# Kernel optimization log

Measured on AMD Instinct MI355X. Metric: run time of the kernel, lower is better.

## Reference

```python
import jax, jax.numpy as jnp
import numpy as np
from jax.scipy.linalg import solve_triangular

JITTER = 1e-5
BIG = 1e9


def _rq(d2, outscale, ls, alpha):
    # Rational-quadratic kernel (gpytorch RQKernel with outputscale)
    return outscale * (1.0 + d2 / (2.0 * alpha * ls * ls)) ** (-alpha)


def _per_var(tb, m, nz, os_, ls, al, K):
    # tb: [L] times of one sample; m: [L] bool, points belonging to this variable.
    # Sequential GP fantasy updates == prefix conditioning. chol of a leading
    # principal block equals leading block of full chol, so one Cholesky +
    # one triangular solve + cumsum over rows reproduces the sequential loop.
    L = tb.shape[0]
    keyt = jnp.where(m, tb, BIG)
    order = jnp.argsort(keyt)            # this variable's points, time-sorted, first
    ts = tb[order]
    ms = m[order]
    mf = ms.astype(tb.dtype)
    d2 = (ts[:, None] - ts[None, :]) ** 2
    Kxx = _rq(d2, os_, ls, al) * (mf[:, None] * mf[None, :])  # masked rows/cols -> 0
    idx = jnp.arange(L)
    # noisy train covariance; masked points get identity rows (decoupled, zero effect)
    Kn = Kxx.at[idx, idx].set(jnp.where(ms, os_ + nz + JITTER, 1.0))
    C = jnp.linalg.cholesky(Kn)
    v = solve_triangular(C, Kxx, lower=True)     # [L train, L test] (test = same points)
    cum = jnp.cumsum(v * v, axis=0)              # variance explained after i obs
    std_pref = jnp.sqrt(jnp.maximum(os_ - cum, 1e-12)) * mf[None, :]
    sums = std_pref.sum(axis=1)                  # sum of posterior stds after each obs
    s0 = jnp.sqrt(os_) * mf.sum()                # prior sum of stds
    prev = jnp.concatenate([s0[None], sums[:-1]])
    gains = jnp.maximum(prev - sums, 0.0) * mf   # info gain per added observation
    # partition timeline into K groups of near-equal total information
    cg = jnp.cumsum(gains)
    frac = (cg - 0.5 * gains) / jnp.maximum(cg[-1], 1e-12)
    grp = jnp.clip(jnp.floor(frac * K), 0, K - 1).astype(jnp.int32)
    return order, mf, grp, gains


def _forward(t, vid, noise, outputscale, lengthscale, alpha, K):
    B, L = t.shape
    V = noise.shape[0]

    def per_bv(tb, vidb, v):
        m = vidb == v
        order, mf, grp, gains = _per_var(tb, m, noise[v], outputscale[v],
                                         lengthscale[v], alpha[v], K)
        col = v * K + grp
        oh = jnp.zeros((L, V * K), t.dtype).at[order, col].add(mf)
        g = jnp.zeros((L,), t.dtype).at[order].add(gains)
        return oh, g

    def per_b(tb, vidb):
        oh, g = jax.vmap(per_bv, in_axes=(None, None, 0))(tb, vidb, jnp.arange(V))
        return oh.sum(0), g.sum(0)   # variables are disjoint -> sum == union

    return jax.vmap(per_b)(t, vid)


def setup_inputs() -> dict:
    key = jax.random.key(0)
    ks = jax.random.split(key, 7)
    B, L, V = 8, 512, 16
    t = jax.random.uniform(ks[0], (B, L), dtype=jnp.float32)
    y = jax.random.normal(ks[1], (B, L), dtype=jnp.float32)
    vid = jax.random.randint(ks[2], (B, L), 0, V, dtype=jnp.int32)
    noise = 0.01 + 0.05 * jax.random.uniform(ks[3], (V,), dtype=jnp.float32)
    outputscale = 0.5 + jax.random.uniform(ks[4], (V,), dtype=jnp.float32)
    lengthscale = 0.05 + 0.2 * jax.random.uniform(ks[5], (V,), dtype=jnp.float32)
    alpha = 0.5 + jax.random.uniform(ks[6], (V,), dtype=jnp.float32)
    return {"t": t, "y": y, "vid": vid, "noise": noise, "outputscale": outputscale,
            "lengthscale": lengthscale, "alpha": alpha, "hyper_num_nodes": 8}


def reference(t, y, vid, noise, outputscale, lengthscale, alpha, hyper_num_nodes):
    # Returns (mask [B, L, V*K] hard one-hot aggregation mask, gains [B, L] info gain).
    # GP posterior variance does not depend on y, so y only affects training (not here).
    mask, gains = _forward(t, vid, noise, outputscale, lengthscale, alpha, hyper_num_nodes)
    return mask, gains
```

## Files before the change

### kernel.cpp

```cpp
#include <hip/hip_runtime.h>
#include <math.h>

#define NMAX 64
#define JITTER 1e-5


__device__ __forceinline__ double rdlane_f64(double x, int lane) {
    union { double d; int i[2]; } a, r;
    a.d = x;
    r.i[0] = __builtin_amdgcn_readlane(a.i[0], lane);
    r.i[1] = __builtin_amdgcn_readlane(a.i[1], lane);
    return r.d;
}

#define FOR16(M) M(0) M(1) M(2) M(3) M(4) M(5) M(6) M(7) \
                 M(8) M(9) M(10) M(11) M(12) M(13) M(14) M(15)

#define FOR16_J(M, Kc) \
    M(Kc,0)  M(Kc,1)  M(Kc,2)  M(Kc,3)  M(Kc,4)  M(Kc,5)  M(Kc,6)  M(Kc,7) \
    M(Kc,8)  M(Kc,9)  M(Kc,10) M(Kc,11) M(Kc,12) M(Kc,13) M(Kc,14) M(Kc,15)

#define LOADT(j) \
    double c##j = ((w16 + j) == lane) ? cdiag : Klds[lane][w16 + j]; \
    double x##j = ((w16 + j) == lane) ? kdiag : Klds[w16 + j][lane];

#define DECLV(j) double v##j = 0.0;

#define FIN(kc, jc) \
    if constexpr ((jc) > (kc)) { \
        double ljk_ = rdlane_f64(c##kc, w16s + jc); \
        c##jc -= c##kc * ljk_; \
        x##jc -= ljk_ * vvk; \
    }

#define FACT(kc) { \
    double dkk = rdlane_f64(c##kc, w16s + kc);   \
    double inv = rsqrt(dkk); \
    c##kc *= inv;                                \
    double vvk = x##kc * inv;                    \
    v##kc = vvk; \
    cum += vvk * vvk; \
    double var_ = os_ - cum; \
    Klds[w16s + kc][lane] = liveC ? sqrt(var_ > 1e-12 ? var_ : 1e-12) : 0.0; \
    FOR16_J(FIN, kc) \
}

#define PUB(j) { panelL[j][lane] = c##j; panelV[j][lane] = v##j; }

#define HOIST(j) \
    const double ml##j  = panelL[j][lane]; \
    const double mvv##j = panelV[j][lane];

#define TRAILK(kc) { \
    const double lk_ = ml##kc; const double vk_ = mvv##kc; \
    const double2 q0_ = *(const double2*)&panelL[kc][w16s + 0]; \
    const double2 q1_ = *(const double2*)&panelL[kc][w16s + 2]; \
    const double2 q2_ = *(const double2*)&panelL[kc][w16s + 4]; \
    const double2 q3_ = *(const double2*)&panelL[kc][w16s + 6]; \
    const double2 q4_ = *(const double2*)&panelL[kc][w16s + 8]; \
    const double2 q5_ = *(const double2*)&panelL[kc][w16s + 10]; \
    const double2 q6_ = *(const double2*)&panelL[kc][w16s + 12]; \
    const double2 q7_ = *(const double2*)&panelL[kc][w16s + 14]; \
    c0  -= lk_ * q0_.x;  x0  -= q0_.x * vk_; \
    c1  -= lk_ * q0_.y;  x1  -= q0_.y * vk_; \
    c2  -= lk_ * q1_.x;  x2  -= q1_.x * vk_; \
    c3  -= lk_ * q1_.y;  x3  -= q1_.y * vk_; \
    c4  -= lk_ * q2_.x;  x4  -= q2_.x * vk_; \
    c5  -= lk_ * q2_.y;  x5  -= q2_.y * vk_; \
    c6  -= lk_ * q3_.x;  x6  -= q3_.x * vk_; \
    c7  -= lk_ * q3_.y;  x7  -= q3_.y * vk_; \
    c8  -= lk_ * q4_.x;  x8  -= q4_.x * vk_; \
    c9  -= lk_ * q4_.y;  x9  -= q4_.y * vk_; \
    c10 -= lk_ * q5_.x;  x10 -= q5_.x * vk_; \
    c11 -= lk_ * q5_.y;  x11 -= q5_.y * vk_; \
    c12 -= lk_ * q6_.x;  x12 -= q6_.x * vk_; \
    c13 -= lk_ * q6_.y;  x13 -= q6_.y * vk_; \
    c14 -= lk_ * q7_.x;  x14 -= q7_.x * vk_; \
    c15 -= lk_ * q7_.y;  x15 -= q7_.y * vk_; \
}

__global__ __attribute__((amdgpu_flat_work_group_size(256, 256), amdgpu_waves_per_eu(1, 1)))
void gp_mask_kernel(const float* __restrict__ t,
                    const int*   __restrict__ vid,
                    const float* __restrict__ noise,
                    const float* __restrict__ outscale,
                    const float* __restrict__ lscale,
                    const float* __restrict__ alpha,
                    const int*   __restrict__ pK,
                    float* __restrict__ out_mask,
                    float* __restrict__ out_gains,
                    int B, int L, int V)
{
    const int b = blockIdx.x / V;
    const int v = blockIdx.x % V;
    const int tid  = threadIdx.x;
    const int lane = tid & 63;
    const int w16  = (tid >> 6) << 4;
    const int w16s = __builtin_amdgcn_readfirstlane(w16);
    const int ws   = w16s >> 4;
    const int Knodes = pK[0];
    const int VK = V * Knodes;

    __shared__ double Klds[NMAX][NMAX + 1];
    __shared__ double panelL[16][NMAX];
    __shared__ double panelV[16][NMAX];
    __shared__ double cumL[NMAX];
    __shared__ double psum[4][NMAX];
    __shared__ double ts[NMAX];
    __shared__ float  tu[NMAX];
    __shared__ int    idx_u[NMAX];
    __shared__ int    oidx[NMAX];
    __shared__ int    cnt;

    if ((Knodes & 3) == 0) {
        const int kq = Knodes >> 2;
        const float4 z = make_float4(0.f, 0.f, 0.f, 0.f);
        for (int q = tid; q < L * kq; q += 256) {
            int p = q / kq, g = q - p * kq;
            float4* dst = (float4*)(out_mask + ((size_t)b * L + p) * VK + v * Knodes) + g;
            *dst = z;
        }
    } else {
        for (int q = tid; q < L * Knodes; q += 256) {
            int p = q / Knodes, g = q - p * Knodes;
            out_mask[((size_t)b * L + p) * VK + v * Knodes + g] = 0.0f;
        }
    }

    if (tid == 0) cnt = 0;
    __syncthreads();

    for (int i = tid; i < L; i += 256) {
        if (vid[b * L + i] == v) {
            int p = atomicAdd(&cnt, 1);
            if (p < NMAX) { idx_u[p] = i; tu[p] = t[b * L + i]; }
        }
    }
    __syncthreads();
    int n = __builtin_amdgcn_readfirstlane(cnt);
    if (n > NMAX) n = NMAX;

    if (tid < n) {
        float tv = tu[tid]; int iv = idx_u[tid];
        int r = 0;
        for (int e = 0; e < n; e++) {
            float te = tu[e]; int ie = idx_u[e];
            if (te < tv || (te == tv && ie < iv)) r++;
        }
        ts[r] = (double)tv;
        oidx[r] = iv;
    }
    __syncthreads();

    const double os_ = (double)outscale[v];
    const double nz  = (double)noise[v];
    const double ls  = (double)lscale[v];
    const double al  = (double)alpha[v];
    const double isc = 1.0 / (2.0 * al * ls * ls);
    const double s_  = nz + JITTER;

    for (int q = tid; q < NMAX * (NMAX + 1); q += 256)
        ((double*)Klds)[q] = 0.0;
    __syncthreads();
    {
        const int P2 = n * (n - 1) / 2;
        for (int e = tid; e < P2; e += 256) {
            int i = (int)((sqrt(8.0 * (double)e + 1.0) + 1.0) * 0.5);
            while (i * (i - 1) / 2 > e) --i;
            while ((i + 1) * i / 2 <= e) ++i;
            int j = e - i * (i - 1) / 2;
            double d = ts[i] - ts[j];
            double val = os_ * pow(1.0 + d * d * isc, -al);
            Klds[i][j] = val;
            Klds[j][i] = val;
        }
    }
    __syncthreads();

    const bool liveC = lane < n;
    const double cdiag = liveC ? (os_ + s_) : 1.0;
    const double kdiag = liveC ? os_ : 0.0;

    FOR16(LOADT)
    FOR16(DECLV)
    __syncthreads();

    const int P = (n + 15) >> 4;
    double cum = 0.0;
    for (int p = 0; p < P; p++) {
        if (ws == p) {
            if (p > 0) cum = cumL[lane];
            FOR16(FACT)
            FOR16(PUB)
            cumL[lane] = cum;
        }
        __syncthreads();
        if (ws > p && ws < P) {
            FOR16(HOIST)
            FOR16(TRAILK)
        }
        __syncthreads();
    }

    {
        double ps = 0.0;
        #pragma unroll
        for (int jj = 0; jj < 16; jj++) ps += Klds[lane][w16 + jj];
        psum[ws][lane] = ps;
    }
    __syncthreads();

    if (tid < 64 && n > 0) {
        double s_mine = psum[0][tid] + psum[1][tid] + psum[2][tid] + psum[3][tid];

        double sprev = __shfl(s_mine, (tid == 0) ? 0 : tid - 1, 64);
        double prev  = (tid == 0) ? sqrt(os_) * (double)n : sprev;
        double g = 0.0;
        if (tid < n) {
            g = prev - s_mine;
            if (g < 0.0) g = 0.0;
        }
        double sc = g;
        #pragma unroll
        for (int off = 1; off < 64; off <<= 1) {
            double o = __shfl_up(sc, off, 64);
            if (tid >= off) sc += o;
        }
        double total = __shfl(sc, n - 1, 64);
        if (tid < n) {
            double denom = total > 1e-12 ? total : 1e-12;
            double frac = (sc - 0.5 * g) / denom;
            int grp = (int)floor(frac * (double)Knodes);
            if (grp < 0) grp = 0;
            if (grp > Knodes - 1) grp = Knodes - 1;
            int pnt = oidx[tid];
            out_mask[((size_t)b * L + pnt) * VK + v * Knodes + grp] = 1.0f;
            out_gains[(size_t)b * L + pnt] = (float)g;
        }
    }
}

extern "C" void kernel_launch(void* const* d_in, const int* in_sizes, int n_in,
                              void* d_out, int out_size, void* d_ws, size_t ws_size,
                              hipStream_t stream)
{
    const float* t     = (const float*)d_in[0];
    const int*   vid   = (const int*)d_in[2];
    const float* noise = (const float*)d_in[3];
    const float* osc   = (const float*)d_in[4];
    const float* ls    = (const float*)d_in[5];
    const float* al    = (const float*)d_in[6];
    const int*   pK    = (const int*)d_in[7];

    const int V = in_sizes[3];
    const int L = 512;
    const int B = in_sizes[0] / L;

    float* out_mask  = (float*)d_out;
    float* out_gains = (float*)d_out + ((size_t)out_size - (size_t)B * L);

    gp_mask_kernel<<<B * V, 256, 0, stream>>>(t, vid, noise, osc, ls, al, pK,
                                              out_mask, out_gains, B, L, V);
}
```

Before: 92.47 us.

## Double-buffer Cholesky panels and overlap std computation with trailing update

```diff
diff --git a/kernel.cpp b/kernel.cpp
--- a/kernel.cpp
+++ b/kernel.cpp
@@ -39,28 +39,31 @@
     c##kc *= inv;                                \
     double vvk = x##kc * inv;                    \
     v##kc = vvk; \
-    cum += vvk * vvk; \
+    FOR16_J(FIN, kc) \
+}
+
+#define PUB(j) { panelL[pb][j][lane] = c##j; panelV[pb][j][lane] = v##j; }
+
+#define STD1(j) { \
+    cum += v##j * v##j; \
     double var_ = os_ - cum; \
-    Klds[w16s + kc][lane] = liveC ? sqrt(var_ > 1e-12 ? var_ : 1e-12) : 0.0; \
-    FOR16_J(FIN, kc) \
-}
-
-#define PUB(j) { panelL[j][lane] = c##j; panelV[j][lane] = v##j; }
+    Klds[w16s + j][lane] = liveC ? sqrt(var_ > 1e-12 ? var_ : 1e-12) : 0.0; \
+}
 
 #define HOIST(j) \
-    const double ml##j  = panelL[j][lane]; \
-    const double mvv##j = panelV[j][lane];
+    const double ml##j  = panelL[pb][j][lane]; \
+    const double mvv##j = panelV[pb][j][lane];
 
 #define TRAILK(kc) { \
     const double lk_ = ml##kc; const double vk_ = mvv##kc; \
-    const double2 q0_ = *(const double2*)&panelL[kc][w16s + 0]; \
-    const double2 q1_ = *(const double2*)&panelL[kc][w16s + 2]; \
-    const double2 q2_ = *(const double2*)&panelL[kc][w16s + 4]; \
-    const double2 q3_ = *(const double2*)&panelL[kc][w16s + 6]; \
-    const double2 q4_ = *(const double2*)&panelL[kc][w16s + 8]; \
-    const double2 q5_ = *(const double2*)&panelL[kc][w16s + 10]; \
-    const double2 q6_ = *(const double2*)&panelL[kc][w16s + 12]; \
-    const double2 q7_ = *(const double2*)&panelL[kc][w16s + 14]; \
+    const double2 q0_ = *(const double2*)&panelL[pb][kc][w16s + 0]; \
+    const double2 q1_ = *(const double2*)&panelL[pb][kc][w16s + 2]; \
+    const double2 q2_ = *(const double2*)&panelL[pb][kc][w16s + 4]; \
+    const double2 q3_ = *(const double2*)&panelL[pb][kc][w16s + 6]; \
+    const double2 q4_ = *(const double2*)&panelL[pb][kc][w16s + 8]; \
+    const double2 q5_ = *(const double2*)&panelL[pb][kc][w16s + 10]; \
+    const double2 q6_ = *(const double2*)&panelL[pb][kc][w16s + 12]; \
+    const double2 q7_ = *(const double2*)&panelL[pb][kc][w16s + 14]; \
     c0  -= lk_ * q0_.x;  x0  -= q0_.x * vk_; \
     c1  -= lk_ * q0_.y;  x1  -= q0_.y * vk_; \
     c2  -= lk_ * q1_.x;  x2  -= q1_.x * vk_; \
@@ -102,8 +105,8 @@
     const int VK = V * Knodes;
 
     __shared__ double Klds[NMAX][NMAX + 1];
-    __shared__ double panelL[16][NMAX];
-    __shared__ double panelV[16][NMAX];
+    __shared__ double panelL[2][16][NMAX];
+    __shared__ double panelV[2][16][NMAX];
     __shared__ double cumL[NMAX];
     __shared__ double psum[4][NMAX];
     __shared__ double ts[NMAX];
@@ -157,6 +160,7 @@
     const double ls  = (double)lscale[v];
     const double al  = (double)alpha[v];
     const double isc = 1.0 / (2.0 * al * ls * ls);
+    const double nal = -al;
     const double s_  = nz + JITTER;
 
     for (int q = tid; q < NMAX * (NMAX + 1); q += 256)
@@ -170,7 +174,8 @@
             while ((i + 1) * i / 2 <= e) ++i;
             int j = e - i * (i - 1) / 2;
             double d = ts[i] - ts[j];
-            double val = os_ * pow(1.0 + d * d * isc, -al);
+            double u = 1.0 + d * d * isc;
+            double val = os_ * exp2(nal * log2(u));
             Klds[i][j] = val;
             Klds[j][i] = val;
         }
@@ -186,21 +191,23 @@
     __syncthreads();
 
     const int P = (n + 15) >> 4;
-    double cum = 0.0;
     for (int p = 0; p < P; p++) {
+        const int pb = p & 1;
         if (ws == p) {
-            if (p > 0) cum = cumL[lane];
             FOR16(FACT)
             FOR16(PUB)
+        }
+        __syncthreads();
+        if (ws == p) {
+            double cum = (p == 0) ? 0.0 : cumL[lane];
+            FOR16(STD1)
             cumL[lane] = cum;
-        }
-        __syncthreads();
-        if (ws > p && ws < P) {
+        } else if (ws > p && ws < P) {
             FOR16(HOIST)
             FOR16(TRAILK)
         }
-        __syncthreads();
-    }
+    }
+    __syncthreads();
 
     {
         double ps = 0.0;
```

Result: faster. 89.20 us (-3.5%).
